# Kernel tuning notes

Measured on AMD Instinct MI355X. Metric: run time of the kernel, lower is better.

Reference implementation:

```python
import jax, jax.numpy as jnp
import numpy as np

H = 1024      # hidden_size
NH = 16       # num_attention_heads
HD = H // NH  # head_size
DF = 4096     # ff intermediate
EPS = 1e-5


def layer_norm(x, g, b):
    mu = jnp.mean(x, axis=-1, keepdims=True)
    var = jnp.var(x, axis=-1, keepdims=True)
    return (x - mu) * jax.lax.rsqrt(var + EPS) * g + b


def setup_inputs() -> dict:
    key = jax.random.key(0)
    ks = jax.random.split(key, 4)
    s = 0.02
    return {
        "x": jax.random.normal(ks[0], (2, 2048, H), dtype=jnp.float32),
        "w_qkv": jax.random.normal(ks[1], (H, 3 * H), dtype=jnp.float32) * s,
        "ln1_g": jnp.ones((H,), jnp.float32),
        "ln1_b": jnp.zeros((H,), jnp.float32),
        "w1": jax.random.normal(ks[2], (H, DF), dtype=jnp.float32) * s,
        "b1": jnp.zeros((DF,), jnp.float32),
        "w2": jax.random.normal(ks[3], (DF, H), dtype=jnp.float32) * s,
        "b2": jnp.zeros((H,), jnp.float32),
        "ln2_g": jnp.ones((H,), jnp.float32),
        "ln2_b": jnp.zeros((H,), jnp.float32),
    }


def reference(x, w_qkv, ln1_g, ln1_b, w1, b1, w2, b2, ln2_g, ln2_b):
    b, s, h = x.shape
    # --- MHSelfAttention (naive) ---
    qkv = x @ w_qkv                                   # [b, s, 3h]
    qkv = qkv.reshape(b, s, 3, NH, HD)
    q, k, v = (jnp.moveaxis(qkv, 2, 0)                # [3, b, s, nh, hd]
               .transpose(0, 1, 3, 2, 4))             # [3, b, nh, s, hd]
    # NOTE: faithful quirk — scaled by sqrt(hidden_size), not head_size
    scores = jnp.einsum('bnqd,bnkd->bnqk', q, k) / jnp.sqrt(jnp.float32(h))
    probs = jax.nn.softmax(scores, axis=-1)
    ctx = jnp.einsum('bnqk,bnkd->bnqd', probs, v)     # [b, nh, s, hd]
    attn_out = ctx.transpose(0, 2, 1, 3).reshape(b, s, h)
    # post-norm residual (dropout = identity in eval)
    x = x + layer_norm(attn_out, ln1_g, ln1_b)
    # --- FFN ---
    ff = jax.nn.relu(x @ w1 + b1) @ w2 + b2
    x = x + layer_norm(ff, ln2_g, ln2_b)
    return x
```

## Files before the change

### kernel.cpp

```cpp
#include <hip/hip_runtime.h>


typedef unsigned short u16;
typedef unsigned int u32;
typedef __bf16 bf16x8 __attribute__((ext_vector_type(8)));
typedef float f32x4 __attribute__((ext_vector_type(4)));
typedef float f32x16 __attribute__((ext_vector_type(16)));
typedef u32 u32x4 __attribute__((ext_vector_type(4)));
typedef u16 u16x4 __attribute__((ext_vector_type(4)));

__device__ __forceinline__ u16 f2b(float f) {
  u32 u = __builtin_bit_cast(u32, f);
  u += 0x7fffu + ((u >> 16) & 1u);
  return (u16)(u >> 16);
}
__device__ __forceinline__ float b2f(u16 u) {
  return __builtin_bit_cast(float, (u32)u << 16);
}

__device__ __forceinline__ u32 cvtpk(float lo, float hi) {
  u32 r;
  asm("v_cvt_pk_bf16_f32 %0, %1, %2" : "=v"(r) : "v"(lo), "v"(hi));
  return r;
}

__device__ __forceinline__ void gld_lds16(const u16* g, u16* l) {
  __builtin_amdgcn_global_load_lds(
      (const __attribute__((address_space(1))) u32*)g,
      (__attribute__((address_space(3))) u32*)l, 16, 0, 0);
}

__device__ __forceinline__ void transpose32(
    const float* __restrict__ in, u16* __restrict__ out, int R, int C,
    int bx, int by, float (*tile)[33], int tid) {
  const int cb = bx * 32, rb = by * 32;
  const int c = tid & 31;
  const int r0 = tid >> 5;
#pragma unroll
  for (int rr = 0; rr < 32; rr += 8)
    tile[r0 + rr][c] = in[(size_t)(rb + r0 + rr) * C + cb + c];
  __syncthreads();
#pragma unroll
  for (int rr = 0; rr < 32; rr += 8)
    out[(size_t)(cb + r0 + rr) * R + rb + c] = f2b(tile[c][r0 + rr]);
}

__global__ __launch_bounds__(256) void prep1_kernel(
    const float* __restrict__ x, u16* __restrict__ xb,
    const float* __restrict__ w_qkv, u16* __restrict__ wqkvT) {
  __shared__ float tile[32][33];
  const int bid = blockIdx.x;
  const int tid = threadIdx.x;
  if (bid < 4096) {
    const int idx = bid * 256 + tid;
    float4 v = ((const float4*)x)[idx];
    u16x4 o = { f2b(v.x), f2b(v.y), f2b(v.z), f2b(v.w) };
    ((u16x4*)xb)[idx] = o;
  } else {
    const int t = bid - 4096;
    transpose32(w_qkv, wqkvT, 1024, 3072, t % 96, t / 96, tile, tid);
  }
}

__global__ __launch_bounds__(256) void prep2_kernel(
    const float* __restrict__ w1, u16* __restrict__ w1T,
    const float* __restrict__ w2, u16* __restrict__ w2T) {
  __shared__ float tile[32][33];
  const int bid = blockIdx.x;
  const int tid = threadIdx.x;
  if (bid < 4096) {
    transpose32(w1, w1T, 1024, 4096, bid % 128, bid / 128, tile, tid);
  } else {
    const int t = bid - 4096;
    transpose32(w2, w2T, 4096, 1024, t % 32, t / 32, tile, tid);
  }
}

__global__ __launch_bounds__(256) void transpose_v_kernel(
    const u16* __restrict__ qkv, u16* __restrict__ vt) {
  __shared__ u16 t[64][70];
  const int bh = blockIdx.x, st = blockIdx.y;
  const int b = bh >> 4, nh = bh & 15;
  const int s0 = st * 64;
  const int r = threadIdx.x >> 3, c = (threadIdx.x & 7) << 3;
  const u16* src = qkv + (size_t)(b * 2048 + s0) * 3072 + 2048 + nh * 64;
#pragma unroll
  for (int rr = 0; rr < 64; rr += 32)
    *(u32x4*)&t[r + rr][c] = *(const u32x4*)(src + (size_t)(r + rr) * 3072 + c);
  __syncthreads();
  u16* dst = vt + ((size_t)bh * 64) * 2048 + s0;
#pragma unroll
  for (int rr = 0; rr < 64; rr += 32) {
    const int d = r + rr;
    u16 tmp[8];
#pragma unroll
    for (int j = 0; j < 8; ++j) tmp[j] = t[c + j][d];
    *(u32x4*)(dst + (size_t)d * 2048 + c) = *(u32x4*)tmp;
  }
}

#define GT(BUF, SBUF, T2, VM)                                                 \
  {                                                                           \
    const u16(*Ab)[32] = As[BUF];                                             \
    const u16(*Bb)[32] = Bs[BUF];                                             \
    bf16x8 af[4], bfr[4];                                                     \
    _Pragma("unroll") for (int nr = 0; nr < 4; ++nr)                          \
        bfr[nr] = *(const bf16x8*)&Bb[wn * 64 + nr * 16 + l16][cRd];          \
    _Pragma("unroll") for (int mr = 0; mr < 4; ++mr)                          \
        af[mr] = *(const bf16x8*)&Ab[wm * 128 + mr * 16 + l16][cRd];          \
    if ((T2) >= 0) {                                                          \
      gld_lds16(Ag + (size_t)(T2) * 32,         &As[SBUF][w * 16][0]);        \
      gld_lds16(Ag + rstep + (size_t)(T2) * 32, &As[SBUF][128 + w * 16][0]);  \
    }                                                                         \
    asm volatile("s_waitcnt lgkmcnt(0)" ::: "memory");                        \
    __builtin_amdgcn_sched_barrier(0);                                        \
    __builtin_amdgcn_s_setprio(1);                                            \
    _Pragma("unroll") for (int mr = 0; mr < 4; ++mr)                          \
        _Pragma("unroll") for (int nr = 0; nr < 4; ++nr)                      \
            acc[mr][nr] = __builtin_amdgcn_mfma_f32_16x16x32_bf16(            \
                af[mr], bfr[nr], acc[mr][nr], 0, 0, 0);                       \
    __builtin_amdgcn_s_setprio(0);                                            \
    _Pragma("unroll") for (int mr = 0; mr < 4; ++mr)                          \
        af[mr] = *(const bf16x8*)&Ab[wm * 128 + 64 + mr * 16 + l16][cRd];     \
    if ((T2) >= 0) {                                                          \
      gld_lds16(Bg + (size_t)(T2) * 32,         &Bs[SBUF][w * 16][0]);        \
      gld_lds16(Bg + rstep + (size_t)(T2) * 32, &Bs[SBUF][128 + w * 16][0]);  \
    }                                                                         \
    asm volatile("s_waitcnt lgkmcnt(0)" ::: "memory");                        \
    __builtin_amdgcn_sched_barrier(0);                                        \
    __builtin_amdgcn_s_setprio(1);                                            \
    _Pragma("unroll") for (int mr = 0; mr < 4; ++mr)                          \
        _Pragma("unroll") for (int nr = 0; nr < 4; ++nr)                      \
            acc[4 + mr][nr] = __builtin_amdgcn_mfma_f32_16x16x32_bf16(        \
                af[mr], bfr[nr], acc[4 + mr][nr], 0, 0, 0);                   \
    __builtin_amdgcn_s_setprio(0);                                            \
    if ((VM) == 4) asm volatile("s_waitcnt vmcnt(4)" ::: "memory");           \
    else if ((VM) == 0) asm volatile("s_waitcnt vmcnt(0)" ::: "memory");      \
    if ((VM) >= 0) __builtin_amdgcn_s_barrier();                              \
  }

__global__ __launch_bounds__(512) void gemm256_kernel(
    const u16* __restrict__ A, const u16* __restrict__ Bt,
    const float* __restrict__ bias, u16* __restrict__ Cb,
    int M, int N, int K, int relu,
    u16* __restrict__ Cb1, u16* __restrict__ Cb2, u16* __restrict__ Cb3) {
  const int nN = N >> 8;
  const int lin = (blockIdx.x & 7) * ((int)gridDim.x >> 3) + (blockIdx.x >> 3);
  const int m0 = (lin / nN) << 8;
  const int n0 = (lin % nN) << 8;
  const int z = blockIdx.y;
  if (z == 1) Cb = Cb1; else if (z == 2) Cb = Cb2; else if (z == 3) Cb = Cb3;

  const int tid = threadIdx.x;
  const int w = tid >> 6, lane = tid & 63;
  const int quad = lane >> 4, l16 = lane & 15;
  const int wm = w >> 2, wn = w & 3;

  __shared__ u16 As[3][256][32];
  __shared__ u16 Bs[3][256][32];

  f32x4 acc[8][4];
#pragma unroll
  for (int i = 0; i < 8; ++i)
#pragma unroll
    for (int j = 0; j < 4; ++j) acc[i][j] = {0.f, 0.f, 0.f, 0.f};

  const int srow = lane >> 2;
  const int scol = (((lane & 3) ^ (srow & 3)) << 3);
  const u16* Ag = A + (size_t)(m0 + w * 16 + srow) * K + (size_t)z * 1024 + scol;
  const u16* Bg = Bt + (size_t)(n0 + w * 16 + srow) * K + (size_t)z * 1024 + scol;
  const size_t rstep = (size_t)128 * K;

  const int cRd = ((quad ^ (l16 & 3)) << 3);

  gld_lds16(Ag,              &As[0][w * 16][0]);
  gld_lds16(Ag + rstep,      &As[0][128 + w * 16][0]);
  gld_lds16(Bg,              &Bs[0][w * 16][0]);
  gld_lds16(Bg + rstep,      &Bs[0][128 + w * 16][0]);
  gld_lds16(Ag + 32,         &As[1][w * 16][0]);
  gld_lds16(Ag + rstep + 32, &As[1][128 + w * 16][0]);
  gld_lds16(Bg + 32,         &Bs[1][w * 16][0]);
  gld_lds16(Bg + rstep + 32, &Bs[1][128 + w * 16][0]);
  asm volatile("s_waitcnt vmcnt(4)" ::: "memory");
  __builtin_amdgcn_s_barrier();

  for (int tt = 0; tt < 10; ++tt) {
    const int t = tt * 3;
    GT(0, 2, t + 2, 4)
    GT(1, 0, t + 3, 4)
    GT(2, 1, t + 4, 4)
  }
  GT(0, 0, -1, 0)
  GT(1, 0, -1, -1)

#pragma unroll
  for (int mr = 0; mr < 8; ++mr) {
    const int row = m0 + wm * 128 + mr * 16 + quad * 4;
#pragma unroll
    for (int nr = 0; nr < 4; ++nr) {
      const int col = n0 + wn * 64 + nr * 16 + l16;
      const float bv = bias ? bias[col] : 0.f;
#pragma unroll
      for (int r = 0; r < 4; ++r) {
        float v = acc[mr][nr][r] + bv;
        if (relu) v = fmaxf(v, 0.f);
        Cb[(size_t)(row + r) * N + col] = f2b(v);
      }
    }
  }
}

__global__ __launch_bounds__(256, 4) void attn_kernel(
    const u16* __restrict__ qkv, const u16* __restrict__ vt,
    float* __restrict__ Op0, float* __restrict__ Op1,
    float* __restrict__ lpart) {
  const int bh = blockIdx.x;
  const int qt = blockIdx.y;
  const int kz = blockIdx.z;
  const int b = bh >> 4, nh = bh & 15;
  const int tid = threadIdx.x;
  const int w = tid >> 6, lane = tid & 63;
  const int l32 = lane & 31, hi = lane >> 5;
  const float c2 = 0.04508422f;

  __shared__ u16 KS[64][64];
  __shared__ u16 VS[64][64];

  const size_t rs = 3072;
  const u16* qbase = qkv + (size_t)b * 2048 * rs + nh * 64;
  const u16* kbase = qbase + 1024;
  const u16* vbase = vt + (size_t)bh * 64 * 2048;
  const int q0 = qt * 128;
  const int k0beg = kz * 1024;

  bf16x8 aq[4];
  {
    const u16* qrow = qbase + (size_t)(q0 + w * 32 + l32) * rs + hi * 8;
#pragma unroll
    for (int ds = 0; ds < 4; ++ds) {
      u32x4 v = *(const u32x4*)(qrow + ds * 16);
      u16 ti[8], to[8];
      *(u32x4*)ti = v;
#pragma unroll
      for (int j = 0; j < 8; ++j) to[j] = f2b(b2f(ti[j]) * c2);
      u32x4 pk = *(u32x4*)to;
      aq[ds] = __builtin_bit_cast(bf16x8, pk);
    }
  }

  f32x16 Oacc[2];
#pragma unroll
  for (int dn = 0; dn < 2; ++dn)
#pragma unroll
    for (int i = 0; i < 16; ++i) Oacc[dn][i] = 0.f;
  float ls[4] = {0.f, 0.f, 0.f, 0.f};

  const int srow = lane >> 3;
  const int scol = ((lane & 7) ^ srow) << 3;

#pragma unroll 1
  for (int t = 0; t < 16; ++t) {
    const int k0 = k0beg + t * 64;
    __syncthreads();
    gld_lds16(kbase + (size_t)(k0 + w * 16 + srow) * rs + scol,       &KS[w * 16][0]);
    gld_lds16(kbase + (size_t)(k0 + w * 16 + 8 + srow) * rs + scol,   &KS[w * 16 + 8][0]);
    gld_lds16(vbase + (size_t)(w * 16 + srow) * 2048 + k0 + scol,     &VS[w * 16][0]);
    gld_lds16(vbase + (size_t)(w * 16 + 8 + srow) * 2048 + k0 + scol, &VS[w * 16 + 8][0]);
    __syncthreads();

    f32x16 S[2];
#pragma unroll
    for (int jt = 0; jt < 2; ++jt)
#pragma unroll
      for (int i = 0; i < 16; ++i) S[jt][i] = 0.f;
#pragma unroll
    for (int jt = 0; jt < 2; ++jt) {
      const int krow = jt * 32 + l32;
#pragma unroll
      for (int ds = 0; ds < 4; ++ds) {
        bf16x8 kv = *(const bf16x8*)&KS[krow][((2 * ds + hi) ^ (krow & 7)) << 3];
        S[jt] = __builtin_amdgcn_mfma_f32_32x32x16_bf16(kv, aq[ds], S[jt], 0, 0, 0);
      }
    }

    bf16x8 pa[4];
#pragma unroll
    for (int jt = 0; jt < 2; ++jt) {
      float p[16];
#pragma unroll
      for (int r = 0; r < 16; ++r) {
        p[r] = exp2f(S[jt][r]);
        ls[r & 3] += p[r];
      }
#pragma unroll
      for (int bq = 0; bq < 2; ++bq) {
        u32 x0 = cvtpk(p[8 * bq + 0], p[8 * bq + 1]);
        u32 y0 = cvtpk(p[8 * bq + 4], p[8 * bq + 5]);
        u32 x1 = cvtpk(p[8 * bq + 2], p[8 * bq + 3]);
        u32 y1 = cvtpk(p[8 * bq + 6], p[8 * bq + 7]);
        asm("v_permlane32_swap_b32 %0, %1" : "+v"(x0), "+v"(y0));
        asm("v_permlane32_swap_b32 %0, %1" : "+v"(x1), "+v"(y1));
        u32x4 dw = {x0, x1, y0, y1};
        pa[2 * jt + bq] = __builtin_bit_cast(bf16x8, dw);
      }
    }

#pragma unroll
    for (int dn = 0; dn < 2; ++dn) {
      const int vrow = dn * 32 + l32;
#pragma unroll
      for (int ks = 0; ks < 4; ++ks) {
        bf16x8 vv = *(const bf16x8*)&VS[vrow][((2 * ks + hi) ^ (vrow & 7)) << 3];
        Oacc[dn] = __builtin_amdgcn_mfma_f32_32x32x16_bf16(pa[ks], vv, Oacc[dn], 0, 0, 0);
      }
    }
  }

  float lsum = (ls[0] + ls[1]) + (ls[2] + ls[3]);
  const float ltot = lsum + __shfl_xor(lsum, 32);

  float* opart = kz ? Op1 : Op0;
  float* obase = opart + (size_t)b * 2048 * 1024 + (size_t)nh * 64;
  float* lbase = lpart + (size_t)kz * 4096 * 16 + (size_t)b * 2048 * 16 + nh;
#pragma unroll
  for (int r = 0; r < 16; ++r) {
    const int qrow = q0 + w * 32 + (r & 3) + 8 * (r >> 2) + 4 * hi;
#pragma unroll
    for (int dn = 0; dn < 2; ++dn)
      obase[(size_t)qrow * 1024 + dn * 32 + l32] = Oacc[dn][r];
  }
  if (lane < 32) lbase[(size_t)(q0 + w * 32 + l32) * 16] = ltot;
}

__global__ __launch_bounds__(256) void ln_attn_kernel(
    const float* __restrict__ O0, const float* __restrict__ O1,
    const float* __restrict__ l0, const float* __restrict__ l1,
    const float* __restrict__ xres, const float* __restrict__ g,
    const float* __restrict__ bb, float* __restrict__ outf,
    u16* __restrict__ outb) {
  const int w = threadIdx.x >> 6, lane = threadIdx.x & 63;
  const int row = blockIdx.x * 4 + w;
  const float4* o0r = (const float4*)(O0 + (size_t)row * 1024);
  const float4* o1r = (const float4*)(O1 + (size_t)row * 1024);
  const float* lp0 = l0 + row * 16;
  const float* lp1 = l1 + row * 16;

  float4 v[4];
  float s = 0.f, s2 = 0.f;
#pragma unroll
  for (int j = 0; j < 4; ++j) {
    const int f = j * 64 + lane;
    const int head = f >> 4;
    const float inv = 1.f / (lp0[head] + lp1[head]);
    float4 a0 = o0r[f];
    float4 a1 = o1r[f];
    v[j].x = (a0.x + a1.x) * inv;
    v[j].y = (a0.y + a1.y) * inv;
    v[j].z = (a0.z + a1.z) * inv;
    v[j].w = (a0.w + a1.w) * inv;
    s  += v[j].x + v[j].y + v[j].z + v[j].w;
    s2 += v[j].x * v[j].x + v[j].y * v[j].y + v[j].z * v[j].z + v[j].w * v[j].w;
  }
#pragma unroll
  for (int off = 32; off > 0; off >>= 1) {
    s += __shfl_xor(s, off);
    s2 += __shfl_xor(s2, off);
  }
  const float mu = s * (1.f / 1024.f);
  const float var = s2 * (1.f / 1024.f) - mu * mu;
  const float rstd = rsqrtf(var + 1e-5f);

  const float4* xr4 = (const float4*)(xres + (size_t)row * 1024);
  float4* of4 = (float4*)(outf + (size_t)row * 1024);
  u16x4* ob4 = (u16x4*)(outb + (size_t)row * 1024);
#pragma unroll
  for (int j = 0; j < 4; ++j) {
    const int f = j * 64 + lane;
    float4 xr = xr4[f];
    float4 gv = ((const float4*)g)[f];
    float4 bv = ((const float4*)bb)[f];
    float4 o;
    o.x = xr.x + (v[j].x - mu) * rstd * gv.x + bv.x;
    o.y = xr.y + (v[j].y - mu) * rstd * gv.y + bv.y;
    o.z = xr.z + (v[j].z - mu) * rstd * gv.z + bv.z;
    o.w = xr.w + (v[j].w - mu) * rstd * gv.w + bv.w;
    of4[f] = o;
    u16x4 ob = { f2b(o.x), f2b(o.y), f2b(o.z), f2b(o.w) };
    ob4[f] = ob;
  }
}

__global__ __launch_bounds__(256) void ln_ffn_kernel(
    const u16* __restrict__ p0, const u16* __restrict__ p1,
    const u16* __restrict__ p2, const u16* __restrict__ p3,
    const float* __restrict__ bias, const float* __restrict__ xres,
    const float* __restrict__ g, const float* __restrict__ bb,
    float* __restrict__ outf) {
  const int w = threadIdx.x >> 6, lane = threadIdx.x & 63;
  const int row = blockIdx.x * 4 + w;
  const u16x4* p0r = (const u16x4*)(p0 + (size_t)row * 1024);
  const u16x4* p1r = (const u16x4*)(p1 + (size_t)row * 1024);
  const u16x4* p2r = (const u16x4*)(p2 + (size_t)row * 1024);
  const u16x4* p3r = (const u16x4*)(p3 + (size_t)row * 1024);

  float4 v[4];
  float s = 0.f, s2 = 0.f;
#pragma unroll
  for (int j = 0; j < 4; ++j) {
    const int f = j * 64 + lane;
    u16x4 a0 = p0r[f];
    u16x4 a1 = p1r[f];
    u16x4 a2 = p2r[f];
    u16x4 a3 = p3r[f];
    float4 bv4 = ((const float4*)bias)[f];
    v[j].x = (b2f(a0[0]) + b2f(a1[0])) + (b2f(a2[0]) + b2f(a3[0])) + bv4.x;
    v[j].y = (b2f(a0[1]) + b2f(a1[1])) + (b2f(a2[1]) + b2f(a3[1])) + bv4.y;
    v[j].z = (b2f(a0[2]) + b2f(a1[2])) + (b2f(a2[2]) + b2f(a3[2])) + bv4.z;
    v[j].w = (b2f(a0[3]) + b2f(a1[3])) + (b2f(a2[3]) + b2f(a3[3])) + bv4.w;
    s  += v[j].x + v[j].y + v[j].z + v[j].w;
    s2 += v[j].x * v[j].x + v[j].y * v[j].y + v[j].z * v[j].z + v[j].w * v[j].w;
  }
#pragma unroll
  for (int off = 32; off > 0; off >>= 1) {
    s += __shfl_xor(s, off);
    s2 += __shfl_xor(s2, off);
  }
  const float mu = s * (1.f / 1024.f);
  const float var = s2 * (1.f / 1024.f) - mu * mu;
  const float rstd = rsqrtf(var + 1e-5f);

  const float4* xr4 = (const float4*)(xres + (size_t)row * 1024);
  float4* of4 = (float4*)(outf + (size_t)row * 1024);
#pragma unroll
  for (int j = 0; j < 4; ++j) {
    const int f = j * 64 + lane;
    float4 xr = xr4[f];
    float4 gv = ((const float4*)g)[f];
    float4 bv = ((const float4*)bb)[f];
    float4 o;
    o.x = xr.x + (v[j].x - mu) * rstd * gv.x + bv.x;
    o.y = xr.y + (v[j].y - mu) * rstd * gv.y + bv.y;
    o.z = xr.z + (v[j].z - mu) * rstd * gv.z + bv.z;
    o.w = xr.w + (v[j].w - mu) * rstd * gv.w + bv.w;
    of4[f] = o;
  }
}

extern "C" void kernel_launch(void* const* d_in, const int* in_sizes, int n_in,
                              void* d_out, int out_size, void* d_ws, size_t ws_size,
                              hipStream_t stream) {
  const float* x     = (const float*)d_in[0];
  const float* w_qkv = (const float*)d_in[1];
  const float* ln1_g = (const float*)d_in[2];
  const float* ln1_b = (const float*)d_in[3];
  const float* w1    = (const float*)d_in[4];
  const float* b1    = (const float*)d_in[5];
  const float* w2    = (const float*)d_in[6];
  const float* b2    = (const float*)d_in[7];
  const float* ln2_g = (const float*)d_in[8];
  const float* ln2_b = (const float*)d_in[9];
  float* out = (float*)d_out;
  char* ws = (char*)d_ws;

  u16*   xb    = (u16*)(ws + 0);
  u16*   wqkvT = (u16*)(ws + 8388608);
  u16*   qkvb  = (u16*)(ws + 31457280);
  u16*   vT    = (u16*)(ws + 56623104);
  float* Op0   = (float*)(ws + 0);
  float* Op1   = (float*)(ws + 73400320);
  float* lp    = (float*)(ws + 90177536);
  float* x1    = (float*)(ws + 31457280);
  u16*   x1b   = (u16*)(ws + 48234496);
  u16*   w1T   = (u16*)(ws + 14680064);
  u16*   w2T   = (u16*)(ws + 23068672);
  u16*   h1    = (u16*)(ws + 56623104);
  u16*   fp0   = (u16*)(ws + 0);
  u16*   fp1   = (u16*)(ws + 8388608);
  u16*   fp2   = (u16*)(ws + 48234496);
  u16*   fp3   = (u16*)(ws + 90177536);

  prep1_kernel<<<7168, 256, 0, stream>>>(x, xb, w_qkv, wqkvT);

  gemm256_kernel<<<dim3(192, 1), 512, 0, stream>>>(
      xb, wqkvT, nullptr, qkvb, 4096, 3072, 1024, 0,
      nullptr, nullptr, nullptr);
  transpose_v_kernel<<<dim3(32, 32), 256, 0, stream>>>(qkvb, vT);
  attn_kernel<<<dim3(32, 16, 2), 256, 0, stream>>>(qkvb, vT, Op0, Op1, lp);

  ln_attn_kernel<<<1024, 256, 0, stream>>>(
      Op0, Op1, lp, lp + 4096 * 16, x, ln1_g, ln1_b, x1, x1b);

  prep2_kernel<<<8192, 256, 0, stream>>>(w1, w1T, w2, w2T);

  gemm256_kernel<<<dim3(256, 1), 512, 0, stream>>>(
      x1b, w1T, b1, h1, 4096, 4096, 1024, 1,
      nullptr, nullptr, nullptr);
  gemm256_kernel<<<dim3(64, 4), 512, 0, stream>>>(
      h1, w2T, nullptr, fp0, 4096, 1024, 4096, 0,
      fp1, fp2, fp3);

  ln_ffn_kernel<<<1024, 256, 0, stream>>>(
      fp0, fp1, fp2, fp3, b2, x1, ln2_g, ln2_b, out);
}
```

Measured before the change: 321.9 us.

## Restructure GEMM mainloop to 64-wide K tiles with double-buffered phased staging

The 256x256 GEMM mainloop moves from 32-wide K tiles in a triple buffer to 64-wide K tiles in a double buffer, with LDS laid out as [half][128][64] and an 8-way XOR swizzle. Each K tile is split into four phases. In each phase a slice of A fragments is read and a few global-to-LDS loads for later tiles are issued before the MFMAs run, and a barrier follows every phase. The aim is to halve the number of loop iterations per K, feed two MFMA K-steps per fragment load, and spread global loads more evenly across compute. The cost is many more barriers per tile and a finer-grained vmcnt scheme that has to be exactly right for correctness.

Result: no change. 323.7 us (+0.6%).

```diff
diff --git a/kernel.cpp b/kernel.cpp
--- a/kernel.cpp
+++ b/kernel.cpp
@@ -99,45 +99,42 @@
   }
 }
 
-#define GT(BUF, SBUF, T2, VM)                                                 \
+
+#define STG_A(D, H, RB, T) \
+  gld_lds16(AgS + (size_t)((H) * 128 + (RB)) * K + (size_t)(T) * 64, &As[D][H][(RB) + w8][0]);
+#define STG_B(D, H, RB, T) \
+  gld_lds16(BgS + (size_t)((H) * 128 + (RB)) * K + (size_t)(T) * 64, &Bs[D][H][(RB) + w8][0]);
+
+#define LDB(D)                                                                \
+  _Pragma("unroll") for (int nr = 0; nr < 4; ++nr)                            \
+    _Pragma("unroll") for (int s = 0; s < 2; ++s)                             \
+      bfr[nr][s] = *(const bf16x8*)&Bs[D][bh_][bn_ + nr * 16 + l16]           \
+                                      [((s * 4 + quad) ^ (l16 & 7)) * 8];
+
+#define PH(D, Q, STAGE, VM)                                                   \
   {                                                                           \
-    const u16(*Ab)[32] = As[BUF];                                             \
-    const u16(*Bb)[32] = Bs[BUF];                                             \
-    bf16x8 af[4], bfr[4];                                                     \
-    _Pragma("unroll") for (int nr = 0; nr < 4; ++nr)                          \
-        bfr[nr] = *(const bf16x8*)&Bb[wn * 64 + nr * 16 + l16][cRd];          \
-    _Pragma("unroll") for (int mr = 0; mr < 4; ++mr)                          \
-        af[mr] = *(const bf16x8*)&Ab[wm * 128 + mr * 16 + l16][cRd];          \
-    if ((T2) >= 0) {                                                          \
-      gld_lds16(Ag + (size_t)(T2) * 32,         &As[SBUF][w * 16][0]);        \
-      gld_lds16(Ag + rstep + (size_t)(T2) * 32, &As[SBUF][128 + w * 16][0]);  \
-    }                                                                         \
+    bf16x8 aqf[2][2];                                                         \
+    _Pragma("unroll") for (int mi = 0; mi < 2; ++mi)                          \
+      _Pragma("unroll") for (int s = 0; s < 2; ++s)                           \
+        aqf[mi][s] = *(const bf16x8*)&As[D][wm][(2 * (Q) + mi) * 16 + l16]    \
+                                        [((s * 4 + quad) ^ (l16 & 7)) * 8];   \
+    STAGE                                                                     \
+    __builtin_amdgcn_s_barrier();                                             \
     asm volatile("s_waitcnt lgkmcnt(0)" ::: "memory");                        \
     __builtin_amdgcn_sched_barrier(0);                                        \
     __builtin_amdgcn_s_setprio(1);                                            \
-    _Pragma("unroll") for (int mr = 0; mr < 4; ++mr)                          \
-        _Pragma("unroll") for (int nr = 0; nr < 4; ++nr)                      \
-            acc[mr][nr] = __builtin_amdgcn_mfma_f32_16x16x32_bf16(            \
-                af[mr], bfr[nr], acc[mr][nr], 0, 0, 0);                       \
+    _Pragma("unroll") for (int mi = 0; mi < 2; ++mi)                          \
+      _Pragma("unroll") for (int nr = 0; nr < 4; ++nr)                        \
+        _Pragma("unroll") for (int s = 0; s < 2; ++s)                         \
+          acc[2 * (Q) + mi][nr] = __builtin_amdgcn_mfma_f32_16x16x32_bf16(    \
+              aqf[mi][s], bfr[nr][s], acc[2 * (Q) + mi][nr], 0, 0, 0);        \
     __builtin_amdgcn_s_setprio(0);                                            \
-    _Pragma("unroll") for (int mr = 0; mr < 4; ++mr)                          \
-        af[mr] = *(const bf16x8*)&Ab[wm * 128 + 64 + mr * 16 + l16][cRd];     \
-    if ((T2) >= 0) {                                                          \
-      gld_lds16(Bg + (size_t)(T2) * 32,         &Bs[SBUF][w * 16][0]);        \
-      gld_lds16(Bg + rstep + (size_t)(T2) * 32, &Bs[SBUF][128 + w * 16][0]);  \
-    }                                                                         \
-    asm volatile("s_waitcnt lgkmcnt(0)" ::: "memory");                        \
-    __builtin_amdgcn_sched_barrier(0);                                        \
-    __builtin_amdgcn_s_setprio(1);                                            \
-    _Pragma("unroll") for (int mr = 0; mr < 4; ++mr)                          \
-        _Pragma("unroll") for (int nr = 0; nr < 4; ++nr)                      \
-            acc[4 + mr][nr] = __builtin_amdgcn_mfma_f32_16x16x32_bf16(        \
-                af[mr], bfr[nr], acc[4 + mr][nr], 0, 0, 0);                   \
-    __builtin_amdgcn_s_setprio(0);                                            \
-    if ((VM) == 4) asm volatile("s_waitcnt vmcnt(4)" ::: "memory");           \
-    else if ((VM) == 0) asm volatile("s_waitcnt vmcnt(0)" ::: "memory");      \
-    if ((VM) >= 0) __builtin_amdgcn_s_barrier();                              \
-  }
+    VM                                                                        \
+    __builtin_amdgcn_s_barrier();                                             \
+  }
+
+#define VM6 asm volatile("s_waitcnt vmcnt(6)" ::: "memory");
+#define VM0 asm volatile("s_waitcnt vmcnt(0)" ::: "memory");
 
 __global__ __launch_bounds__(512) void gemm256_kernel(
     const u16* __restrict__ A, const u16* __restrict__ Bt,
@@ -155,9 +152,10 @@
   const int w = tid >> 6, lane = tid & 63;
   const int quad = lane >> 4, l16 = lane & 15;
   const int wm = w >> 2, wn = w & 3;
-
-  __shared__ u16 As[3][256][32];
-  __shared__ u16 Bs[3][256][32];
+  const int bh_ = wn >> 1, bn_ = (wn & 1) * 64;
+
+  __shared__ u16 As[2][2][128][64];
+  __shared__ u16 Bs[2][2][128][64];
 
   f32x4 acc[8][4];
 #pragma unroll
@@ -165,33 +163,44 @@
 #pragma unroll
     for (int j = 0; j < 4; ++j) acc[i][j] = {0.f, 0.f, 0.f, 0.f};
 
-  const int srow = lane >> 2;
-  const int scol = (((lane & 3) ^ (srow & 3)) << 3);
-  const u16* Ag = A + (size_t)(m0 + w * 16 + srow) * K + (size_t)z * 1024 + scol;
-  const u16* Bg = Bt + (size_t)(n0 + w * 16 + srow) * K + (size_t)z * 1024 + scol;
-  const size_t rstep = (size_t)128 * K;
-
-  const int cRd = ((quad ^ (l16 & 3)) << 3);
-
-  gld_lds16(Ag,              &As[0][w * 16][0]);
-  gld_lds16(Ag + rstep,      &As[0][128 + w * 16][0]);
-  gld_lds16(Bg,              &Bs[0][w * 16][0]);
-  gld_lds16(Bg + rstep,      &Bs[0][128 + w * 16][0]);
-  gld_lds16(Ag + 32,         &As[1][w * 16][0]);
-  gld_lds16(Ag + rstep + 32, &As[1][128 + w * 16][0]);
-  gld_lds16(Bg + 32,         &Bs[1][w * 16][0]);
-  gld_lds16(Bg + rstep + 32, &Bs[1][128 + w * 16][0]);
-  asm volatile("s_waitcnt vmcnt(4)" ::: "memory");
+  const int sr8 = lane >> 3;
+  const int sc8 = ((lane & 7) ^ sr8) << 3;
+  const int w8 = w * 8;
+  const u16* AgS = A + (size_t)(m0 + w8 + sr8) * K + (size_t)z * 1024 + sc8;
+  const u16* BgS = Bt + (size_t)(n0 + w8 + sr8) * K + (size_t)z * 1024 + sc8;
+
+  bf16x8 bfr[4][2];
+
+  STG_B(0, 0, 0, 0)  STG_B(0, 0, 64, 0)  STG_B(0, 1, 0, 0)  STG_B(0, 1, 64, 0)
+  STG_A(0, 0, 0, 0)  STG_A(0, 1, 0, 0)   STG_A(0, 0, 64, 0) STG_A(0, 1, 64, 0)
+  STG_B(1, 0, 0, 1)  STG_B(1, 0, 64, 1)  STG_B(1, 1, 0, 1)  STG_B(1, 1, 64, 1)
+  STG_A(1, 0, 0, 1)  STG_A(1, 1, 0, 1)
+  asm volatile("s_waitcnt vmcnt(0)" ::: "memory");
   __builtin_amdgcn_s_barrier();
 
-  for (int tt = 0; tt < 10; ++tt) {
-    const int t = tt * 3;
-    GT(0, 2, t + 2, 4)
-    GT(1, 0, t + 3, 4)
-    GT(2, 1, t + 4, 4)
-  }
-  GT(0, 0, -1, 0)
-  GT(1, 0, -1, -1)
+  for (int i = 0; i < 7; ++i) {
+    const int t1 = 2 * i + 1, t2 = 2 * i + 2, t3 = 2 * i + 3;
+    LDB(0)
+    PH(0, 0, STG_A(1, 0, 64, t1) STG_A(1, 1, 64, t1), )
+    PH(0, 1, STG_B(0, 0, 0, t2) STG_B(0, 0, 64, t2), )
+    PH(0, 2, STG_B(0, 1, 0, t2) STG_B(0, 1, 64, t2), )
+    PH(0, 3, STG_A(0, 0, 0, t2) STG_A(0, 1, 0, t2), VM6)
+    LDB(1)
+    PH(1, 0, STG_A(0, 0, 64, t2) STG_A(0, 1, 64, t2), )
+    PH(1, 1, STG_B(1, 0, 0, t3) STG_B(1, 0, 64, t3), )
+    PH(1, 2, STG_B(1, 1, 0, t3) STG_B(1, 1, 64, t3), )
+    PH(1, 3, STG_A(1, 0, 0, t3) STG_A(1, 1, 0, t3), VM6)
+  }
+  LDB(0)
+  PH(0, 0, STG_A(1, 0, 64, 15) STG_A(1, 1, 64, 15), )
+  PH(0, 1, , )
+  PH(0, 2, , )
+  PH(0, 3, , VM0)
+  LDB(1)
+  PH(1, 0, , )
+  PH(1, 1, , )
+  PH(1, 2, , )
+  PH(1, 3, , )
 
 #pragma unroll
   for (int mr = 0; mr < 8; ++mr) {
```

## Add specialized 256x192-tile QKV GEMM kernel to fill all CUs

Applied to the files above, without the earlier changes.

Replaces the generic 256x256-tile GEMM for the QKV projection with a dedicated kernel that uses 256x192 tiles, giving 256 workgroups instead of 192 so the grid maps onto the 256 CUs of the MI355X. It keeps the triple-buffered LDS pipeline with split A/B loads, adapts the wait counts to the uneven B-tile load (only half the waves load the second B strip), and adds a blockIdx swizzle for L2 locality. The cost is smaller per-block reuse and some per-wave load imbalance.

New measurement: 308.4 us. -4.2%, faster.

```diff
diff --git a/kernel.cpp b/kernel.cpp
--- a/kernel.cpp
+++ b/kernel.cpp
@@ -206,6 +206,114 @@
         if (relu) v = fmaxf(v, 0.f);
         Cb[(size_t)(row + r) * N + col] = f2b(v);
       }
+    }
+  }
+}
+
+#define QVM4                                                                  \
+  if (w < 4) { asm volatile("s_waitcnt vmcnt(4)" ::: "memory"); }             \
+  else       { asm volatile("s_waitcnt vmcnt(3)" ::: "memory"); }
+#define QGT(BUF, SBUF, T2, VM)                                                \
+  {                                                                           \
+    const u16(*Ab)[32] = As[BUF];                                             \
+    const u16(*Bb)[32] = Bs[BUF];                                             \
+    bf16x8 af[4], bfr[3];                                                     \
+    _Pragma("unroll") for (int nr = 0; nr < 3; ++nr)                          \
+        bfr[nr] = *(const bf16x8*)&Bb[wn * 48 + nr * 16 + l16][cRd];          \
+    _Pragma("unroll") for (int mr = 0; mr < 4; ++mr)                          \
+        af[mr] = *(const bf16x8*)&Ab[wm * 128 + mr * 16 + l16][cRd];          \
+    if ((T2) >= 0) {                                                          \
+      gld_lds16(Ag + (size_t)(T2) * 32,         &As[SBUF][w * 16][0]);        \
+      gld_lds16(Ag + rstep + (size_t)(T2) * 32, &As[SBUF][128 + w * 16][0]);  \
+    }                                                                         \
+    asm volatile("s_waitcnt lgkmcnt(0)" ::: "memory");                        \
+    __builtin_amdgcn_sched_barrier(0);                                        \
+    __builtin_amdgcn_s_setprio(1);                                            \
+    _Pragma("unroll") for (int mr = 0; mr < 4; ++mr)                          \
+        _Pragma("unroll") for (int nr = 0; nr < 3; ++nr)                      \
+            acc[mr][nr] = __builtin_amdgcn_mfma_f32_16x16x32_bf16(            \
+                af[mr], bfr[nr], acc[mr][nr], 0, 0, 0);                       \
+    __builtin_amdgcn_s_setprio(0);                                            \
+    _Pragma("unroll") for (int mr = 0; mr < 4; ++mr)                          \
+        af[mr] = *(const bf16x8*)&Ab[wm * 128 + 64 + mr * 16 + l16][cRd];     \
+    if ((T2) >= 0) {                                                          \
+      gld_lds16(Bg + (size_t)(T2) * 32,         &Bs[SBUF][w * 16][0]);        \
+      if (w < 4)                                                              \
+        gld_lds16(Bg2 + (size_t)(T2) * 32,      &Bs[SBUF][128 + w * 16][0]);  \
+    }                                                                         \
+    asm volatile("s_waitcnt lgkmcnt(0)" ::: "memory");                        \
+    __builtin_amdgcn_sched_barrier(0);                                        \
+    __builtin_amdgcn_s_setprio(1);                                            \
+    _Pragma("unroll") for (int mr = 0; mr < 4; ++mr)                          \
+        _Pragma("unroll") for (int nr = 0; nr < 3; ++nr)                      \
+            acc[4 + mr][nr] = __builtin_amdgcn_mfma_f32_16x16x32_bf16(        \
+                af[mr], bfr[nr], acc[4 + mr][nr], 0, 0, 0);                   \
+    __builtin_amdgcn_s_setprio(0);                                            \
+    if ((VM) == 4) { QVM4 }                                                   \
+    else if ((VM) == 0) asm volatile("s_waitcnt vmcnt(0)" ::: "memory");      \
+    if ((VM) >= 0) __builtin_amdgcn_s_barrier();                              \
+  }
+
+__global__ __launch_bounds__(512) void gemm_qkv_kernel(
+    const u16* __restrict__ A, const u16* __restrict__ Bt,
+    u16* __restrict__ Cb) {
+  const int K = 1024, N = 3072;
+  const int lin = (blockIdx.x & 7) * 32 + (blockIdx.x >> 3);
+  const int m0 = (lin >> 4) << 8;
+  const int n0 = (lin & 15) * 192;
+
+  const int tid = threadIdx.x;
+  const int w = tid >> 6, lane = tid & 63;
+  const int quad = lane >> 4, l16 = lane & 15;
+  const int wm = w >> 2, wn = w & 3;
+
+  __shared__ u16 As[3][256][32];
+  __shared__ u16 Bs[3][192][32];
+
+  f32x4 acc[8][3];
+#pragma unroll
+  for (int i = 0; i < 8; ++i)
+#pragma unroll
+    for (int j = 0; j < 3; ++j) acc[i][j] = {0.f, 0.f, 0.f, 0.f};
+
+  const int srow = lane >> 2;
+  const int scol = (((lane & 3) ^ (srow & 3)) << 3);
+  const u16* Ag = A + (size_t)(m0 + w * 16 + srow) * K + scol;
+  const u16* Bg = Bt + (size_t)(n0 + w * 16 + srow) * K + scol;
+  const u16* Bg2 = Bt + (size_t)(n0 + 128 + w * 16 + srow) * K + scol;
+  const size_t rstep = (size_t)128 * K;
+
+  const int cRd = ((quad ^ (l16 & 3)) << 3);
+
+  gld_lds16(Ag,              &As[0][w * 16][0]);
+  gld_lds16(Ag + rstep,      &As[0][128 + w * 16][0]);
+  gld_lds16(Bg,              &Bs[0][w * 16][0]);
+  if (w < 4) gld_lds16(Bg2,  &Bs[0][128 + w * 16][0]);
+  gld_lds16(Ag + 32,         &As[1][w * 16][0]);
+  gld_lds16(Ag + rstep + 32, &As[1][128 + w * 16][0]);
+  gld_lds16(Bg + 32,         &Bs[1][w * 16][0]);
+  if (w < 4) gld_lds16(Bg2 + 32, &Bs[1][128 + w * 16][0]);
+  QVM4
+  __builtin_amdgcn_s_barrier();
+
+  for (int tt = 0; tt < 10; ++tt) {
+    const int t = tt * 3;
+    QGT(0, 2, t + 2, 4)
+    QGT(1, 0, t + 3, 4)
+    QGT(2, 1, t + 4, 4)
+  }
+  QGT(0, 0, -1, 0)
+  QGT(1, 0, -1, -1)
+
+#pragma unroll
+  for (int mr = 0; mr < 8; ++mr) {
+    const int row = m0 + wm * 128 + mr * 16 + quad * 4;
+#pragma unroll
+    for (int nr = 0; nr < 3; ++nr) {
+      const int col = n0 + wn * 48 + nr * 16 + l16;
+#pragma unroll
+      for (int r = 0; r < 4; ++r)
+        Cb[(size_t)(row + r) * N + col] = f2b(acc[mr][nr][r]);
     }
   }
 }
@@ -481,9 +589,7 @@
 
   prep1_kernel<<<7168, 256, 0, stream>>>(x, xb, w_qkv, wqkvT);
 
-  gemm256_kernel<<<dim3(192, 1), 512, 0, stream>>>(
-      xb, wqkvT, nullptr, qkvb, 4096, 3072, 1024, 0,
-      nullptr, nullptr, nullptr);
+  gemm_qkv_kernel<<<256, 512, 0, stream>>>(xb, wqkvT, qkvb);
   transpose_v_kernel<<<dim3(32, 32), 256, 0, stream>>>(qkvb, vT);
   attn_kernel<<<dim3(32, 16, 2), 256, 0, stream>>>(qkvb, vT, Op0, Op1, lp);
 
```

## Use 16-wave GEMM blocks and a 256x192 tiled QKV GEMM for full CU coverage

Applied to the files above, without the earlier changes.

The 256x256 GEMM now runs with 1024 threads (16 waves), each wave computing a 64x64 sub-tile, so it issues half the loads and MFMAs per wave with a single compute phase per k-step. A new QKV GEMM uses 256x192 tiles, so the 4096x3072 problem maps to 256 blocks instead of 192, matching the CU count better. Only 12 of the 16 waves load B tiles, so the vmcnt waits differ per wave. Per-wave register pressure drops, but MFMA issue per wave shrinks and there are more waves competing at each barrier.

New measurement: 303.9 us. 1.06x faster.

```diff
diff --git a/kernel.cpp b/kernel.cpp
--- a/kernel.cpp
+++ b/kernel.cpp
@@ -99,7 +99,7 @@
   }
 }
 
-#define GT(BUF, SBUF, T2, VM)                                                 \
+#define GT16(BUF, SBUF, T2, VM)                                               \
   {                                                                           \
     const u16(*Ab)[32] = As[BUF];                                             \
     const u16(*Bb)[32] = Bs[BUF];                                             \
@@ -107,10 +107,10 @@
     _Pragma("unroll") for (int nr = 0; nr < 4; ++nr)                          \
         bfr[nr] = *(const bf16x8*)&Bb[wn * 64 + nr * 16 + l16][cRd];          \
     _Pragma("unroll") for (int mr = 0; mr < 4; ++mr)                          \
-        af[mr] = *(const bf16x8*)&Ab[wm * 128 + mr * 16 + l16][cRd];          \
+        af[mr] = *(const bf16x8*)&Ab[wm * 64 + mr * 16 + l16][cRd];           \
     if ((T2) >= 0) {                                                          \
-      gld_lds16(Ag + (size_t)(T2) * 32,         &As[SBUF][w * 16][0]);        \
-      gld_lds16(Ag + rstep + (size_t)(T2) * 32, &As[SBUF][128 + w * 16][0]);  \
+      gld_lds16(Ag + (size_t)(T2) * 32, &As[SBUF][w * 16][0]);                \
+      gld_lds16(Bg + (size_t)(T2) * 32, &Bs[SBUF][w * 16][0]);                \
     }                                                                         \
     asm volatile("s_waitcnt lgkmcnt(0)" ::: "memory");                        \
     __builtin_amdgcn_sched_barrier(0);                                        \
@@ -120,26 +120,12 @@
             acc[mr][nr] = __builtin_amdgcn_mfma_f32_16x16x32_bf16(            \
                 af[mr], bfr[nr], acc[mr][nr], 0, 0, 0);                       \
     __builtin_amdgcn_s_setprio(0);                                            \
-    _Pragma("unroll") for (int mr = 0; mr < 4; ++mr)                          \
-        af[mr] = *(const bf16x8*)&Ab[wm * 128 + 64 + mr * 16 + l16][cRd];     \
-    if ((T2) >= 0) {                                                          \
-      gld_lds16(Bg + (size_t)(T2) * 32,         &Bs[SBUF][w * 16][0]);        \
-      gld_lds16(Bg + rstep + (size_t)(T2) * 32, &Bs[SBUF][128 + w * 16][0]);  \
-    }                                                                         \
-    asm volatile("s_waitcnt lgkmcnt(0)" ::: "memory");                        \
-    __builtin_amdgcn_sched_barrier(0);                                        \
-    __builtin_amdgcn_s_setprio(1);                                            \
-    _Pragma("unroll") for (int mr = 0; mr < 4; ++mr)                          \
-        _Pragma("unroll") for (int nr = 0; nr < 4; ++nr)                      \
-            acc[4 + mr][nr] = __builtin_amdgcn_mfma_f32_16x16x32_bf16(        \
-                af[mr], bfr[nr], acc[4 + mr][nr], 0, 0, 0);                   \
-    __builtin_amdgcn_s_setprio(0);                                            \
-    if ((VM) == 4) asm volatile("s_waitcnt vmcnt(4)" ::: "memory");           \
+    if ((VM) == 2) asm volatile("s_waitcnt vmcnt(2)" ::: "memory");           \
     else if ((VM) == 0) asm volatile("s_waitcnt vmcnt(0)" ::: "memory");      \
     if ((VM) >= 0) __builtin_amdgcn_s_barrier();                              \
   }
 
-__global__ __launch_bounds__(512) void gemm256_kernel(
+__global__ __launch_bounds__(1024) void gemm256_kernel(
     const u16* __restrict__ A, const u16* __restrict__ Bt,
     const float* __restrict__ bias, u16* __restrict__ Cb,
     int M, int N, int K, int relu,
@@ -159,9 +145,9 @@
   __shared__ u16 As[3][256][32];
   __shared__ u16 Bs[3][256][32];
 
-  f32x4 acc[8][4];
-#pragma unroll
-  for (int i = 0; i < 8; ++i)
+  f32x4 acc[4][4];
+#pragma unroll
+  for (int i = 0; i < 4; ++i)
 #pragma unroll
     for (int j = 0; j < 4; ++j) acc[i][j] = {0.f, 0.f, 0.f, 0.f};
 
@@ -169,33 +155,28 @@
   const int scol = (((lane & 3) ^ (srow & 3)) << 3);
   const u16* Ag = A + (size_t)(m0 + w * 16 + srow) * K + (size_t)z * 1024 + scol;
   const u16* Bg = Bt + (size_t)(n0 + w * 16 + srow) * K + (size_t)z * 1024 + scol;
-  const size_t rstep = (size_t)128 * K;
 
   const int cRd = ((quad ^ (l16 & 3)) << 3);
 
-  gld_lds16(Ag,              &As[0][w * 16][0]);
-  gld_lds16(Ag + rstep,      &As[0][128 + w * 16][0]);
-  gld_lds16(Bg,              &Bs[0][w * 16][0]);
-  gld_lds16(Bg + rstep,      &Bs[0][128 + w * 16][0]);
-  gld_lds16(Ag + 32,         &As[1][w * 16][0]);
-  gld_lds16(Ag + rstep + 32, &As[1][128 + w * 16][0]);
-  gld_lds16(Bg + 32,         &Bs[1][w * 16][0]);
-  gld_lds16(Bg + rstep + 32, &Bs[1][128 + w * 16][0]);
-  asm volatile("s_waitcnt vmcnt(4)" ::: "memory");
+  gld_lds16(Ag,      &As[0][w * 16][0]);
+  gld_lds16(Bg,      &Bs[0][w * 16][0]);
+  gld_lds16(Ag + 32, &As[1][w * 16][0]);
+  gld_lds16(Bg + 32, &Bs[1][w * 16][0]);
+  asm volatile("s_waitcnt vmcnt(2)" ::: "memory");
   __builtin_amdgcn_s_barrier();
 
   for (int tt = 0; tt < 10; ++tt) {
     const int t = tt * 3;
-    GT(0, 2, t + 2, 4)
-    GT(1, 0, t + 3, 4)
-    GT(2, 1, t + 4, 4)
-  }
-  GT(0, 0, -1, 0)
-  GT(1, 0, -1, -1)
-
-#pragma unroll
-  for (int mr = 0; mr < 8; ++mr) {
-    const int row = m0 + wm * 128 + mr * 16 + quad * 4;
+    GT16(0, 2, t + 2, 2)
+    GT16(1, 0, t + 3, 2)
+    GT16(2, 1, t + 4, 2)
+  }
+  GT16(0, 0, -1, 0)
+  GT16(1, 0, -1, -1)
+
+#pragma unroll
+  for (int mr = 0; mr < 4; ++mr) {
+    const int row = m0 + wm * 64 + mr * 16 + quad * 4;
 #pragma unroll
     for (int nr = 0; nr < 4; ++nr) {
       const int col = n0 + wn * 64 + nr * 16 + l16;
@@ -206,6 +187,94 @@
         if (relu) v = fmaxf(v, 0.f);
         Cb[(size_t)(row + r) * N + col] = f2b(v);
       }
+    }
+  }
+}
+
+#define QVMC                                                                  \
+  if (w < 12) { asm volatile("s_waitcnt vmcnt(2)" ::: "memory"); }            \
+  else        { asm volatile("s_waitcnt vmcnt(1)" ::: "memory"); }
+#define QGT16(BUF, SBUF, T2, VM)                                              \
+  {                                                                           \
+    const u16(*Ab)[32] = As[BUF];                                             \
+    const u16(*Bb)[32] = Bs[BUF];                                             \
+    bf16x8 af[4], bfr[3];                                                     \
+    _Pragma("unroll") for (int nr = 0; nr < 3; ++nr)                          \
+        bfr[nr] = *(const bf16x8*)&Bb[wn * 48 + nr * 16 + l16][cRd];          \
+    _Pragma("unroll") for (int mr = 0; mr < 4; ++mr)                          \
+        af[mr] = *(const bf16x8*)&Ab[wm * 64 + mr * 16 + l16][cRd];           \
+    if ((T2) >= 0) {                                                          \
+      gld_lds16(Ag + (size_t)(T2) * 32, &As[SBUF][w * 16][0]);                \
+      if (w < 12)                                                             \
+        gld_lds16(Bg + (size_t)(T2) * 32, &Bs[SBUF][w * 16][0]);              \
+    }                                                                         \
+    asm volatile("s_waitcnt lgkmcnt(0)" ::: "memory");                        \
+    __builtin_amdgcn_sched_barrier(0);                                        \
+    __builtin_amdgcn_s_setprio(1);                                            \
+    _Pragma("unroll") for (int mr = 0; mr < 4; ++mr)                          \
+        _Pragma("unroll") for (int nr = 0; nr < 3; ++nr)                      \
+            acc[mr][nr] = __builtin_amdgcn_mfma_f32_16x16x32_bf16(            \
+                af[mr], bfr[nr], acc[mr][nr], 0, 0, 0);                       \
+    __builtin_amdgcn_s_setprio(0);                                            \
+    if ((VM) == 2) { QVMC }                                                   \
+    else if ((VM) == 0) asm volatile("s_waitcnt vmcnt(0)" ::: "memory");      \
+    if ((VM) >= 0) __builtin_amdgcn_s_barrier();                              \
+  }
+
+__global__ __launch_bounds__(1024) void gemm_qkv_kernel(
+    const u16* __restrict__ A, const u16* __restrict__ Bt,
+    u16* __restrict__ Cb) {
+  const int K = 1024, N = 3072;
+  const int lin = (blockIdx.x & 7) * 32 + (blockIdx.x >> 3);
+  const int m0 = (lin >> 4) << 8;
+  const int n0 = (lin & 15) * 192;
+
+  const int tid = threadIdx.x;
+  const int w = tid >> 6, lane = tid & 63;
+  const int quad = lane >> 4, l16 = lane & 15;
+  const int wm = w >> 2, wn = w & 3;
+
+  __shared__ u16 As[3][256][32];
+  __shared__ u16 Bs[3][192][32];
+
+  f32x4 acc[4][3];
+#pragma unroll
+  for (int i = 0; i < 4; ++i)
+#pragma unroll
+    for (int j = 0; j < 3; ++j) acc[i][j] = {0.f, 0.f, 0.f, 0.f};
+
+  const int srow = lane >> 2;
+  const int scol = (((lane & 3) ^ (srow & 3)) << 3);
+  const u16* Ag = A + (size_t)(m0 + w * 16 + srow) * K + scol;
+  const u16* Bg = Bt + (size_t)(n0 + w * 16 + srow) * K + scol;
+
+  const int cRd = ((quad ^ (l16 & 3)) << 3);
+
+  gld_lds16(Ag,      &As[0][w * 16][0]);
+  if (w < 12) gld_lds16(Bg,      &Bs[0][w * 16][0]);
+  gld_lds16(Ag + 32, &As[1][w * 16][0]);
+  if (w < 12) gld_lds16(Bg + 32, &Bs[1][w * 16][0]);
+  QVMC
+  __builtin_amdgcn_s_barrier();
+
+  for (int tt = 0; tt < 10; ++tt) {
+    const int t = tt * 3;
+    QGT16(0, 2, t + 2, 2)
+    QGT16(1, 0, t + 3, 2)
+    QGT16(2, 1, t + 4, 2)
+  }
+  QGT16(0, 0, -1, 0)
+  QGT16(1, 0, -1, -1)
+
+#pragma unroll
+  for (int mr = 0; mr < 4; ++mr) {
+    const int row = m0 + wm * 64 + mr * 16 + quad * 4;
+#pragma unroll
+    for (int nr = 0; nr < 3; ++nr) {
+      const int col = n0 + wn * 48 + nr * 16 + l16;
+#pragma unroll
+      for (int r = 0; r < 4; ++r)
+        Cb[(size_t)(row + r) * N + col] = f2b(acc[mr][nr][r]);
     }
   }
 }
@@ -481,9 +550,7 @@
 
   prep1_kernel<<<7168, 256, 0, stream>>>(x, xb, w_qkv, wqkvT);
 
-  gemm256_kernel<<<dim3(192, 1), 512, 0, stream>>>(
-      xb, wqkvT, nullptr, qkvb, 4096, 3072, 1024, 0,
-      nullptr, nullptr, nullptr);
+  gemm_qkv_kernel<<<256, 1024, 0, stream>>>(xb, wqkvT, qkvb);
   transpose_v_kernel<<<dim3(32, 32), 256, 0, stream>>>(qkvb, vT);
   attn_kernel<<<dim3(32, 16, 2), 256, 0, stream>>>(qkvb, vT, Op0, Op1, lp);
 
@@ -492,10 +559,10 @@
 
   prep2_kernel<<<8192, 256, 0, stream>>>(w1, w1T, w2, w2T);
 
-  gemm256_kernel<<<dim3(256, 1), 512, 0, stream>>>(
+  gemm256_kernel<<<dim3(256, 1), 1024, 0, stream>>>(
       x1b, w1T, b1, h1, 4096, 4096, 1024, 1,
       nullptr, nullptr, nullptr);
-  gemm256_kernel<<<dim3(64, 4), 512, 0, stream>>>(
+  gemm256_kernel<<<dim3(64, 4), 1024, 0, stream>>>(
       h1, w2T, nullptr, fp0, 4096, 1024, 4096, 0,
       fp1, fp2, fp3);
 
```
